# Optimization experiments

Measured on AMD Instinct MI355X. Metric: run time of the kernel, lower is better.

## Reference

```python
import jax, jax.numpy as jnp
import numpy as np

NUM_CLASSES = 26
IGNORE_LABEL = 0
LAMBDA_SMOOTH = 1.0
EPSILON = 1e-05
# static indices of valid (non-ignored) classes
_VALID = np.array([c for c in range(NUM_CLASSES) if c != IGNORE_LABEL])


def setup_inputs() -> dict:
    key = jax.random.key(0)
    k1, k2, k3 = jax.random.split(key, 3)
    B, D, H, W = 1, 160, 192, 224
    fixed_label_map = jax.random.randint(k1, (B, D, H, W), 0, NUM_CLASSES, dtype=jnp.int32)
    warped_moving_label_map = jax.random.randint(k2, (B, D, H, W), 0, NUM_CLASSES, dtype=jnp.int32)
    vector_field = jax.random.normal(k3, (B, 3, D, H, W), dtype=jnp.float32)
    return {
        'fixed_label_map': fixed_label_map,
        'warped_moving_label_map': warped_moving_label_map,
        'vector_field': vector_field,
    }


def _soft_dice(fixed, moving):
    # Equivalent to one-hot expansion + sum over (B,D,H,W), but computed
    # directly from integer labels via histogram counts (single pass).
    f = fixed.reshape(-1)
    m = moving.reshape(-1)
    fixed_vol = jnp.bincount(f, length=NUM_CLASSES).astype(jnp.float32)
    moving_vol = jnp.bincount(m, length=NUM_CLASSES).astype(jnp.float32)
    # intersection[c] = #{voxels: f==c and m==c}
    inter = jnp.bincount(f, weights=(f == m).astype(jnp.float32), length=NUM_CLASSES)
    dice = (2.0 * inter + EPSILON) / (fixed_vol + moving_vol + EPSILON)
    return 1.0 - dice[_VALID].mean()


def _diffusion(vf):
    # vf: [B, 3, D, H, W]
    dz = vf[:, :, 1:, :, :] - vf[:, :, :-1, :, :]
    dy = vf[:, :, :, 1:, :] - vf[:, :, :, :-1, :]
    dx = vf[:, :, :, :, 1:] - vf[:, :, :, :, :-1]
    return (jnp.mean(dz * dz) + jnp.mean(dy * dy) + jnp.mean(dx * dx)) / 3.0


def reference(fixed_label_map, warped_moving_label_map, vector_field):
    similarity_loss = _soft_dice(fixed_label_map, warped_moving_label_map)
    smoothness_loss = _diffusion(vector_field)
    total_loss = similarity_loss + LAMBDA_SMOOTH * smoothness_loss
    return (total_loss, similarity_loss, smoothness_loss)
```

## Files before the change

kernel.cpp:

```cpp
#include <hip/hip_runtime.h>


namespace {
constexpr int NC    = 26;
constexpr int Dd    = 160, Hh = 192, Ww = 224;
constexpr int W4    = Ww / 4;
constexpr int PL4   = Hh * W4;
constexpr int N4L   = Dd * Hh * Ww / 4;
constexpr int JSTRIDE = 33;
constexpr int NBINS   = NC * JSTRIDE;
constexpr int HIST_BLOCKS = 960;
constexpr int HIST_ITERS  = 7;
constexpr int SLAB    = 3;
constexpr int SLABS   = Hh / SLAB;
constexpr int SGRPS   = SLABS / 4;
constexpr int DCH     = 10;
constexpr int DCHUNKS = Dd / DCH;
constexpr int DIFF_BLOCKS = 3 * DCHUNKS * SGRPS;
}

typedef __attribute__((address_space(1))) const void* gva_t;
typedef __attribute__((address_space(3))) void* lva_t;

__global__ void init_ws_kernel(unsigned int* __restrict__ joint,
                               double* __restrict__ sums) {
    int i = blockIdx.x * blockDim.x + threadIdx.x;
    if (i < NBINS) joint[i] = 0u;
    if (i < 3)     sums[i]  = 0.0;
}

__global__ __launch_bounds__(256) void hist_kernel(
        const int4* __restrict__ f4,
        const int4* __restrict__ m4,
        unsigned int* __restrict__ gj) {
    __shared__ int4 sf[256];
    __shared__ int4 sm[256];
    __shared__ unsigned int h[NBINS];
    for (int i = threadIdx.x; i < NBINS; i += 256) h[i] = 0u;

    const int wid = threadIdx.x >> 6;
    int base = blockIdx.x * (HIST_ITERS * 256);

    for (int it = 0; it < HIST_ITERS; ++it) {
        __builtin_amdgcn_global_load_lds((gva_t)(f4 + base + threadIdx.x),
                                         (lva_t)(sf + wid * 64), 16, 0, 0);
        __builtin_amdgcn_global_load_lds((gva_t)(m4 + base + threadIdx.x),
                                         (lva_t)(sm + wid * 64), 16, 0, 0);
        __syncthreads();
        int4 a = sf[threadIdx.x];
        int4 b = sm[threadIdx.x];
        atomicAdd(&h[a.x * JSTRIDE + b.x], 1u);
        atomicAdd(&h[a.y * JSTRIDE + b.y], 1u);
        atomicAdd(&h[a.z * JSTRIDE + b.z], 1u);
        atomicAdd(&h[a.w * JSTRIDE + b.w], 1u);
        __syncthreads();
        base += 256;
    }

    for (int i = threadIdx.x; i < NBINS; i += 256) {
        unsigned int v = h[i];
        if (v) atomicAdd(&gj[i], v);
    }
}

__global__ __launch_bounds__(256, 3) void diff_kernel(
        const float4* __restrict__ v4,
        double* __restrict__ gs) {
    __shared__ float4 halo[4][W4];
    __shared__ float px[4], py[4], pz[4];

    const int lane = threadIdx.x & 63;
    const int wid  = threadIdx.x >> 6;
    const int b    = blockIdx.x;
    const int c      = b / (DCHUNKS * SGRPS);
    const int rem    = b % (DCHUNKS * SGRPS);
    const int dchunk = rem / SGRPS;
    const int sgrp   = rem % SGRPS;
    const int slab   = sgrp * 4 + wid;
    const int h0     = slab * SLAB;
    const int d0     = dchunk * DCH;
    const bool al    = (lane < W4);
    const bool hv    = (slab < SLABS - 1);
    const int  l     = al ? lane : (W4 - 1);

    size_t cur = ((size_t)(c * Dd + d0) * Hh + h0) * W4 + l;

    float4 p0 = v4[cur];
    float4 p1 = v4[cur + W4];
    float4 p2 = v4[cur + 2 * W4];

    float sx = 0.f, sy = 0.f, sz = 0.f;

    for (int k = 0; k < DCH; ++k) {
        const bool dzv = (d0 + k < Dd - 1);
        if (al) halo[wid][lane] = p0;
        float4 hl = p2;
        if (wid == 3 && hv) hl = v4[cur + SLAB * W4];
        float4 n0 = p0, n1 = p1, n2 = p2;
        if (dzv) {
            n0 = v4[cur + PL4];
            n1 = v4[cur + PL4 + W4];
            n2 = v4[cur + PL4 + 2 * W4];
        }
        __syncthreads();
        if (wid < 3) hl = halo[wid + 1][l];

#define DX(P)                                                                  \
        {                                                                      \
            float d1 = (P).y - (P).x, d2 = (P).z - (P).y, d3 = (P).w - (P).z;  \
            sx += d1 * d1 + d2 * d2 + d3 * d3;                                 \
            float nx = __shfl_down((P).x, 1);                                  \
            float d4 = nx - (P).w;                                             \
            sx += (lane < W4 - 1) ? d4 * d4 : 0.f;                             \
        }
        DX(p0) DX(p1) DX(p2)
#undef DX
#define DY(A, B)                                                               \
        {                                                                      \
            float e0 = (B).x - (A).x, e1 = (B).y - (A).y;                      \
            float e2 = (B).z - (A).z, e3 = (B).w - (A).w;                      \
            sy += e0 * e0 + e1 * e1 + e2 * e2 + e3 * e3;                       \
        }
        DY(p0, p1) DY(p1, p2)
        if (hv) DY(p2, hl)
#undef DY
        if (dzv) {
#define DZ(A, B)                                                               \
            {                                                                  \
                float e0 = (B).x - (A).x, e1 = (B).y - (A).y;                  \
                float e2 = (B).z - (A).z, e3 = (B).w - (A).w;                  \
                sz += e0 * e0 + e1 * e1 + e2 * e2 + e3 * e3;                   \
            }
            DZ(p0, n0) DZ(p1, n1) DZ(p2, n2)
#undef DZ
        }
        __syncthreads();
        p0 = n0; p1 = n1; p2 = n2;
        cur += PL4;
    }

    if (!al) { sx = 0.f; sy = 0.f; sz = 0.f; }

    #pragma unroll
    for (int off = 32; off > 0; off >>= 1) {
        sx += __shfl_down(sx, off);
        sy += __shfl_down(sy, off);
        sz += __shfl_down(sz, off);
    }
    if (lane == 0) { px[wid] = sx; py[wid] = sy; pz[wid] = sz; }
    __syncthreads();
    if (threadIdx.x == 0) {
        atomicAdd(&gs[0], (double)(px[0] + px[1] + px[2] + px[3]));
        atomicAdd(&gs[1], (double)(py[0] + py[1] + py[2] + py[3]));
        atomicAdd(&gs[2], (double)(pz[0] + pz[1] + pz[2] + pz[3]));
    }
}

__global__ void finalize_kernel(const unsigned int* __restrict__ gj,
                                const double* __restrict__ gs,
                                float* __restrict__ out) {
    int lane = threadIdx.x & 63;
    float term = 0.f;
    if (lane >= 1 && lane < NC) {
        float fv = 0.f, mv = 0.f;
        #pragma unroll
        for (int m = 0; m < NC; ++m) fv += (float)gj[lane * JSTRIDE + m];
        #pragma unroll
        for (int f = 0; f < NC; ++f) mv += (float)gj[f * JSTRIDE + lane];
        float iv = (float)gj[lane * JSTRIDE + lane];
        term = (2.f * iv + 1e-5f) / (fv + mv + 1e-5f);
    }
    #pragma unroll
    for (int off = 32; off > 0; off >>= 1) term += __shfl_down(term, off);
    if (threadIdx.x == 0 && blockIdx.x == 0) {
        float sim = 1.f - term * (1.f / 25.f);
        double mdx = gs[0] / ((double)3 * Dd * Hh * (Ww - 1));
        double mdy = gs[1] / ((double)3 * Dd * (Hh - 1) * Ww);
        double mdz = gs[2] / ((double)3 * (Dd - 1) * Hh * Ww);
        float smooth = (float)((mdx + mdy + mdz) / 3.0);
        out[0] = sim + smooth;
        out[1] = sim;
        out[2] = smooth;
    }
}

extern "C" void kernel_launch(void* const* d_in, const int* in_sizes, int n_in,
                              void* d_out, int out_size, void* d_ws, size_t ws_size,
                              hipStream_t stream) {
    const int*   fl = (const int*)d_in[0];
    const int*   ml = (const int*)d_in[1];
    const float* vf = (const float*)d_in[2];
    float* out = (float*)d_out;

    unsigned int* joint = (unsigned int*)d_ws;
    double*       sums  = (double*)((char*)d_ws + 3584);

    init_ws_kernel<<<1, 1024, 0, stream>>>(joint, sums);
    hist_kernel<<<HIST_BLOCKS, 256, 0, stream>>>((const int4*)fl, (const int4*)ml, joint);
    diff_kernel<<<DIFF_BLOCKS, 256, 0, stream>>>((const float4*)vf, sums);
    finalize_kernel<<<1, 64, 0, stream>>>(joint, sums, out);
}
```

Baseline: 207.8 us.

## Software-pipeline histogram loads per wave with vmcnt waits instead of block barriers

The joint-histogram kernel now gives each wave its own 4-deep ring of LDS buffers and keeps three global_load_lds tiles in flight, waiting on vmcnt counters instead of two __syncthreads per iteration. Work per block changes from 7 block-wide tiles to 8 tiles per wave, spread over 840 blocks. The goal is to hide global load latency and remove barrier stalls in this memory-bound pass. It relies on raw s_waitcnt encodings and on global_load_lds visibility within a wave without an LDS wait, which is fragile.

```diff
diff --git a/kernel.cpp b/kernel.cpp
--- a/kernel.cpp
+++ b/kernel.cpp
@@ -9,8 +9,8 @@
 constexpr int N4L   = Dd * Hh * Ww / 4;
 constexpr int JSTRIDE = 33;
 constexpr int NBINS   = NC * JSTRIDE;
-constexpr int HIST_BLOCKS = 960;
-constexpr int HIST_ITERS  = 7;
+constexpr int HIST_BLOCKS = 840;
+constexpr int TILES_PER_WAVE = 8;
 constexpr int SLAB    = 3;
 constexpr int SLABS   = Hh / SLAB;
 constexpr int SGRPS   = SLABS / 4;
@@ -22,6 +22,8 @@
 typedef __attribute__((address_space(1))) const void* gva_t;
 typedef __attribute__((address_space(3))) void* lva_t;
 
+#define WAITVM(n) __builtin_amdgcn_s_waitcnt(0x0F70 | (n))
+
 __global__ void init_ws_kernel(unsigned int* __restrict__ joint,
                                double* __restrict__ sums) {
     int i = blockIdx.x * blockDim.x + threadIdx.x;
@@ -33,30 +35,45 @@
         const int4* __restrict__ f4,
         const int4* __restrict__ m4,
         unsigned int* __restrict__ gj) {
-    __shared__ int4 sf[256];
-    __shared__ int4 sm[256];
+    __shared__ int4 fbuf[4][4][64];
+    __shared__ int4 mbuf[4][4][64];
     __shared__ unsigned int h[NBINS];
     for (int i = threadIdx.x; i < NBINS; i += 256) h[i] = 0u;
-
-    const int wid = threadIdx.x >> 6;
-    int base = blockIdx.x * (HIST_ITERS * 256);
-
-    for (int it = 0; it < HIST_ITERS; ++it) {
-        __builtin_amdgcn_global_load_lds((gva_t)(f4 + base + threadIdx.x),
-                                         (lva_t)(sf + wid * 64), 16, 0, 0);
-        __builtin_amdgcn_global_load_lds((gva_t)(m4 + base + threadIdx.x),
-                                         (lva_t)(sm + wid * 64), 16, 0, 0);
-        __syncthreads();
-        int4 a = sf[threadIdx.x];
-        int4 b = sm[threadIdx.x];
+    __syncthreads();
+
+    const int lane = threadIdx.x & 63;
+    const int wid  = threadIdx.x >> 6;
+    const int base = blockIdx.x * 2048 + wid * 512;
+
+#define ISSUE(T)                                                               \
+    __builtin_amdgcn_global_load_lds((gva_t)(f4 + base + (T) * 64 + lane),     \
+                                     (lva_t)&fbuf[wid][(T) & 3][0], 16, 0, 0); \
+    __builtin_amdgcn_global_load_lds((gva_t)(m4 + base + (T) * 64 + lane),     \
+                                     (lva_t)&mbuf[wid][(T) & 3][0], 16, 0, 0);
+
+    ISSUE(0) ISSUE(1) ISSUE(2)
+
+    #pragma unroll
+    for (int it = 0; it < TILES_PER_WAVE; ++it) {
+        if (it + 3 < TILES_PER_WAVE) { ISSUE(it + 3) }
+        const int newer = ((it + 4 < TILES_PER_WAVE) ? (it + 4)
+                                                     : TILES_PER_WAVE) - 1 - it;
+        switch (2 * newer) {
+            case 6: WAITVM(6); break;
+            case 4: WAITVM(4); break;
+            case 2: WAITVM(2); break;
+            default: WAITVM(0); break;
+        }
+        int4 a = fbuf[wid][it & 3][lane];
+        int4 b = mbuf[wid][it & 3][lane];
         atomicAdd(&h[a.x * JSTRIDE + b.x], 1u);
         atomicAdd(&h[a.y * JSTRIDE + b.y], 1u);
         atomicAdd(&h[a.z * JSTRIDE + b.z], 1u);
         atomicAdd(&h[a.w * JSTRIDE + b.w], 1u);
-        __syncthreads();
-        base += 256;
-    }
-
+    }
+#undef ISSUE
+
+    __syncthreads();
     for (int i = threadIdx.x; i < NBINS; i += 256) {
         unsigned int v = h[i];
         if (v) atomicAdd(&gj[i], v);
```

Result: no change. 205.1 us (-1.3%).
